# Performance work log

Hardware: AMD Instinct MI355X
Metric: run time of the kernel (lower is better)

The kernel has to match this reference:

```python
import jax, jax.numpy as jnp
import numpy as np

B, T, IN, OUT = 8, 2048, 1024, 512
DT, TAU = 1.0, 20.0


def setup_inputs() -> dict:
    key = jax.random.key(0)
    k1, k2 = jax.random.split(key)
    x = jax.random.normal(k1, (B, T, IN), jnp.float32)
    lim = 1.0 / np.sqrt(IN)
    weight = jax.random.uniform(k2, (OUT, IN), jnp.float32, -lim, lim)
    bias = jnp.zeros((OUT,), jnp.float32)
    # fixed tau trainer: decay = exp(-dt / tau) per output feature
    decay = jnp.full((OUT,), float(np.exp(-DT / TAU)), jnp.float32)
    return {"input_tensor": x, "weight": weight, "bias": bias, "decay": decay}


def reference(input_tensor, weight, bias, decay):
    # Hoist the time-invariant GEMM out of the recurrence: [B,T,OUT]
    current = jnp.einsum('bti,oi->bto', input_tensor, weight) + bias
    v0 = jnp.zeros((input_tensor.shape[0], weight.shape[0]), input_tensor.dtype)

    def step(v_tm1, c_t):
        v_t = decay * v_tm1 + (1.0 - decay) * c_t
        return v_t, v_t

    # scan over time axis: [T,B,OUT]
    _, outs = jax.lax.scan(step, v0, jnp.swapaxes(current, 0, 1))
    outputs = jnp.swapaxes(outs, 0, 1)  # [B,T,OUT]
    states = jnp.concatenate([v0[:, None, :], outputs], axis=1)[None]  # [1,B,T+1,OUT]
    return outputs, states
```

## Files before the change

### kernel.cpp

```cpp
#include <hip/hip_runtime.h>
#include <hip/hip_bf16.h>
#include <cstddef>
#include <cstdint>

#define BB    8
#define TT    2048
#define KIN   1024
#define NOUT  512
#define CHUNK 32
#define NCHUNK (TT / CHUNK)

#define BM 128
#define BN 128
#define BK 64
#define NKSTEP (KIN / BK)
#define NPAGE  (KIN / 32)
#define TILEB 8192

typedef __attribute__((ext_vector_type(4))) float          f32x4;
typedef __attribute__((ext_vector_type(4))) unsigned int   u32x4;
typedef _Float16 f16x8 __attribute__((ext_vector_type(8)));

__global__ __launch_bounds__(256) void conv_tiled_f16(
    const float* __restrict__ src, unsigned char* __restrict__ dst, int total) {
  int idx = blockIdx.x * blockDim.x + threadIdx.x;
  const int stride = gridDim.x * blockDim.x;
  for (; idx < total; idx += stride) {
    const int r  = idx >> 7;
    const int s8 = idx & 127;
    const float* p = src + (size_t)r * KIN + s8 * 8;
    float4 a = *reinterpret_cast<const float4*>(p);
    float4 b = *reinterpret_cast<const float4*>(p + 4);
    f16x8 h;
    h[0] = (_Float16)a.x; h[1] = (_Float16)a.y;
    h[2] = (_Float16)a.z; h[3] = (_Float16)a.w;
    h[4] = (_Float16)b.x; h[5] = (_Float16)b.y;
    h[6] = (_Float16)b.z; h[7] = (_Float16)b.w;
    const int row  = r & 127;
    const int page = (r >> 7) * NPAGE + (s8 >> 2);
    const int slot = (s8 & 3) ^ ((row >> 1) & 3);
    *reinterpret_cast<f16x8*>(dst + (size_t)page * TILEB + row * 64 + slot * 16) = h;
  }
}

#define G2L(gp, sp)                                                        \
  __builtin_amdgcn_global_load_lds(                                       \
      (const __attribute__((address_space(1))) void*)(gp),                \
      (__attribute__((address_space(3))) void*)(sp), 16, 0, 0)

__global__ __launch_bounds__(256, 2) void gemm_f16(
    const float* __restrict__ X, const unsigned char* __restrict__ Wt,
    const float* __restrict__ bias, const float* __restrict__ decay,
    unsigned short* __restrict__ Cws, float* __restrict__ vend) {
  __shared__ __align__(16) unsigned char smem[32768 + 16384];

  const int tid  = threadIdx.x;
  const int wave = tid >> 6;
  const int lane = tid & 63;
  const int m0 = blockIdx.x * BM;
  const int n0 = blockIdx.y * BN;
  const int wm = (wave >> 1) * 64;
  const int wn = (wave & 1) * 64;
  const int frow = lane & 15;
  const int g    = lane >> 4;

  unsigned char* sA = smem;
  unsigned char* sB = smem + 32768;

  const int arow4 = wave * 4 + (lane >> 4);
  const int aslot = lane & 15;
  const float* gA = X + (size_t)(m0 + arow4) * KIN + ((aslot ^ (arow4 & 7)) << 2);
  const int ldsw = wave * 1024;

  const unsigned char* srcB = Wt + (size_t)(n0 >> 7) * NPAGE * TILEB + tid * 16;

  const int arswz = frow & 7;
  const int swzr  = (g ^ ((frow >> 1) & 3)) << 4;

  f32x4 acc[4][4] = {};

  for (int t = 0; t < NKSTEP; ++t) {
    __syncthreads();
    const int k0 = t * BK;
#pragma unroll
    for (int q = 0; q < 8; ++q)
      G2L(gA + (size_t)(q * 16) * KIN + k0, sA + q * 4096 + ldsw);
    const size_t boff = (size_t)(2 * t) * TILEB;
#pragma unroll
    for (int q = 0; q < 4; ++q)
      G2L(srcB + boff + q * 4096, sB + q * 4096 + ldsw);
    __syncthreads();

#pragma unroll
    for (int kk = 0; kk < 2; ++kk) {
      f16x8 af[4];
#pragma unroll
      for (int mi = 0; mi < 4; ++mi) {
        const int row = wm + mi * 16 + frow;
        const unsigned char* ap = sA + row * 256;
        const int ks0 = kk * 8 + g * 2;
        f32x4 q0 = *reinterpret_cast<const f32x4*>(ap + ((ks0    ) ^ arswz) * 16);
        f32x4 q1 = *reinterpret_cast<const f32x4*>(ap + ((ks0 + 1) ^ arswz) * 16);
        u32x4 hv;
        hv[0] = __builtin_bit_cast(unsigned int, __builtin_amdgcn_cvt_pkrtz(q0[0], q0[1]));
        hv[1] = __builtin_bit_cast(unsigned int, __builtin_amdgcn_cvt_pkrtz(q0[2], q0[3]));
        hv[2] = __builtin_bit_cast(unsigned int, __builtin_amdgcn_cvt_pkrtz(q1[0], q1[1]));
        hv[3] = __builtin_bit_cast(unsigned int, __builtin_amdgcn_cvt_pkrtz(q1[2], q1[3]));
        af[mi] = __builtin_bit_cast(f16x8, hv);
      }
#pragma unroll
      for (int ni = 0; ni < 4; ++ni) {
        f16x8 bf = *reinterpret_cast<const f16x8*>(
            sB + kk * 8192 + (wn + ni * 16 + frow) * 64 + swzr);
#pragma unroll
        for (int mi = 0; mi < 4; ++mi)
          acc[mi][ni] = __builtin_amdgcn_mfma_f32_16x16x32_f16(af[mi], bf, acc[mi][ni], 0, 0, 0);
      }
    }
  }

  const int colb = n0 + wn + frow;
  const int rowb = m0 + wm + (g << 2);
  float bv[4];
#pragma unroll
  for (int ni = 0; ni < 4; ++ni) bv[ni] = bias[colb + ni * 16];
#pragma unroll
  for (int mi = 0; mi < 4; ++mi) {
#pragma unroll
    for (int r = 0; r < 4; ++r) {
#pragma unroll
      for (int ni = 0; ni < 4; ++ni) {
        const _Float16 hv = (_Float16)(acc[mi][ni][r] + bv[ni]);
        Cws[(size_t)(rowb + mi * 16 + r) * NOUT + colb + ni * 16] =
            __builtin_bit_cast(unsigned short, hv);
      }
    }
  }

  {
    float rlo[4], rhi[4];
#pragma unroll
    for (int ni = 0; ni < 4; ++ni) {
      const float d  = decay[colb + ni * 16];
      const float bb = bv[ni];
      const float omd = 1.0f - d;
      const float dd = d * d, d4 = dd * dd, d8 = d4 * d4;
      const float d16 = d8 * d8, d12 = d8 * d4;
      const float dpg = (g == 0) ? d12 : (g == 1) ? d8 : (g == 2) ? d4 : 1.0f;
      float s[4];
#pragma unroll
      for (int mi = 0; mi < 4; ++mi) {
        float v = acc[mi][ni][0] + bb;
        v = v * d + (acc[mi][ni][1] + bb);
        v = v * d + (acc[mi][ni][2] + bb);
        v = v * d + (acc[mi][ni][3] + bb);
        s[mi] = omd * v;
      }
      float ulo = dpg * (s[0] * d16 + s[1]);
      float uhi = dpg * (s[2] * d16 + s[3]);
      ulo += __shfl_xor(ulo, 16); ulo += __shfl_xor(ulo, 32);
      uhi += __shfl_xor(uhi, 16); uhi += __shfl_xor(uhi, 32);
      rlo[ni] = ulo; rhi[ni] = uhi;
    }
    const int b   = m0 >> 11;
    const int clo = ((m0 & (TT - 1)) >> 5) + (wm >> 5);
    const int chunk = clo + (g >> 1);
    const int half  = g >> 1;
    const int nia   = g & 1;
    const float v1 = half ? (nia ? rhi[1] : rhi[0]) : (nia ? rlo[1] : rlo[0]);
    const float v2 = half ? (nia ? rhi[3] : rhi[2]) : (nia ? rlo[3] : rlo[2]);
    const int col1 = n0 + wn + frow + nia * 16;
    float* vp = vend + ((size_t)b * NCHUNK + chunk) * NOUT;
    vp[col1]      = v1;
    vp[col1 + 32] = v2;
  }
}

__global__ __launch_bounds__(256) void gemm_f32_64x64(
    const float* __restrict__ X, const float* __restrict__ W,
    const float* __restrict__ bias, float* __restrict__ C) {
  __shared__ float As[16][65];
  __shared__ float Bs[16][65];
  const int m0  = blockIdx.y * 64;
  const int n0  = blockIdx.x * 64;
  const int tid = threadIdx.x;
  const int tx  = tid & 15;
  const int ty  = tid >> 4;
  const int lr  = tid >> 2;
  const int lk  = (tid & 3) << 2;
  float acc[4][4] = {};
  const float* xa = X + (size_t)(m0 + lr) * KIN + lk;
  const float* wb = W + (size_t)(n0 + lr) * KIN + lk;
  for (int k0 = 0; k0 < KIN; k0 += 16) {
    float4 av = *reinterpret_cast<const float4*>(xa + k0);
    float4 bv = *reinterpret_cast<const float4*>(wb + k0);
    As[lk + 0][lr] = av.x; As[lk + 1][lr] = av.y;
    As[lk + 2][lr] = av.z; As[lk + 3][lr] = av.w;
    Bs[lk + 0][lr] = bv.x; Bs[lk + 1][lr] = bv.y;
    Bs[lk + 2][lr] = bv.z; Bs[lk + 3][lr] = bv.w;
    __syncthreads();
#pragma unroll
    for (int k = 0; k < 16; ++k) {
      float a[4], b[4];
#pragma unroll
      for (int i = 0; i < 4; ++i) a[i] = As[k][ty * 4 + i];
#pragma unroll
      for (int j = 0; j < 4; ++j) b[j] = Bs[k][tx * 4 + j];
#pragma unroll
      for (int i = 0; i < 4; ++i)
#pragma unroll
        for (int j = 0; j < 4; ++j) acc[i][j] += a[i] * b[j];
    }
    __syncthreads();
  }
  const int n = n0 + tx * 4;
  float4 bv = *reinterpret_cast<const float4*>(&bias[n]);
#pragma unroll
  for (int i = 0; i < 4; ++i) {
    const int m = m0 + ty * 4 + i;
    float4 r;
    r.x = acc[i][0] + bv.x; r.y = acc[i][1] + bv.y;
    r.z = acc[i][2] + bv.z; r.w = acc[i][3] + bv.w;
    *reinterpret_cast<float4*>(&C[(size_t)m * NOUT + n]) = r;
  }
}

__global__ __launch_bounds__(512) void scan_fixup2(
    const unsigned short* __restrict__ Cws, const float* __restrict__ vend,
    const float* __restrict__ decay, float* __restrict__ out,
    float* __restrict__ states) {
  const int b = blockIdx.x / NCHUNK;
  const int c = blockIdx.x % NCHUNK;
  const int o = threadIdx.x;
  const float d   = decay[o];
  const float omd = 1.0f - d;
  const float dd = d * d, d4 = dd * dd, d8 = d4 * d4, d16 = d8 * d8;
  const float dL = d16 * d16;

  float v = 0.0f;
  const float* vp = vend + (size_t)b * NCHUNK * NOUT + o;
  for (int cc = 0; cc < c; ++cc) v = dL * v + vp[(size_t)cc * NOUT];

  size_t obase = ((size_t)b * TT + (size_t)c * CHUNK) * NOUT + o;
  size_t sbase = ((size_t)b * (TT + 1) + (size_t)c * CHUNK + 1) * NOUT + o;
#pragma unroll 4
  for (int k = 0; k < CHUNK; ++k) {
    const unsigned short hu = Cws[obase + (size_t)k * NOUT];
    const float cur = (float)__builtin_bit_cast(_Float16, hu);
    v = d * v + omd * cur;
    out[obase + (size_t)k * NOUT]    = v;
    states[sbase + (size_t)k * NOUT] = v;
  }
  if (c == 0) states[((size_t)b * (TT + 1)) * NOUT + o] = 0.0f;
}

__global__ __launch_bounds__(512) void scan_seq(
    float* __restrict__ C, float* __restrict__ states,
    const float* __restrict__ decay) {
  const int b = blockIdx.x;
  const int o = threadIdx.x;
  const float d   = decay[o];
  const float omd = 1.0f - d;
  float v = 0.0f;
  states[((size_t)b * (TT + 1)) * NOUT + o] = 0.0f;
  for (int t = 0; t < TT; ++t) {
    const size_t oi = ((size_t)b * TT + t) * NOUT + o;
    float x = C[oi];
    v = d * v + omd * x;
    C[oi] = v;
    states[((size_t)b * (TT + 1) + t + 1) * NOUT + o] = v;
  }
}

extern "C" void kernel_launch(void* const* d_in, const int* in_sizes, int n_in,
                              void* d_out, int out_size, void* d_ws, size_t ws_size,
                              hipStream_t stream) {
  const float* x     = (const float*)d_in[0];
  const float* w     = (const float*)d_in[1];
  const float* bias  = (const float*)d_in[2];
  const float* decay = (const float*)d_in[3];

  float* out    = (float*)d_out;
  float* states = out + (size_t)BB * TT * NOUT;

  const size_t szWb = (size_t)NOUT * KIN * sizeof(_Float16);
  const size_t szCb = (size_t)BB * TT * NOUT * sizeof(_Float16);
  const size_t scan_elems = (size_t)BB * NCHUNK * NOUT;
  const size_t need = szWb + szCb + scan_elems * sizeof(float);

  if (ws_size >= need) {
    unsigned char*  Wt   = (unsigned char*)d_ws;
    unsigned short* Cws  = (unsigned short*)(Wt + szWb);
    float*          vend = (float*)(Cws + (size_t)BB * TT * NOUT);

    conv_tiled_f16<<<256, 256, 0, stream>>>(w, Wt, NOUT * (KIN / 8));
    gemm_f16<<<dim3((BB * TT) / BM, NOUT / BN), 256, 0, stream>>>(
        x, Wt, bias, decay, Cws, vend);
    scan_fixup2<<<BB * NCHUNK, NOUT, 0, stream>>>(Cws, vend, decay, out, states);
  } else {
    gemm_f32_64x64<<<dim3(NOUT / 64, (BB * TT) / 64), 256, 0, stream>>>(x, w, bias, out);
    scan_seq<<<BB, NOUT, 0, stream>>>(out, states, decay);
  }
}
```

Before: 62.16 us.

## Fuse GEMM and chunked scan into one cooperative kernel with grid sync

Merges the GEMM and the scan fixup into a single cooperative kernel. After each tile writes its chunk-end partial sums, a grid-wide sync runs, and each wave then computes its chunk prefix and finishes the recurrence straight from accumulators staged in LDS. This removes the fp16 intermediate round trip through global memory and one kernel launch. In exchange it needs all 512 blocks co-resident (128x4 grid at 2 blocks/CU with 64KB LDS), adds a grid barrier, and serialises 64 timesteps per lane with strided stores. If the cooperative launch fails, it falls back to the old two-kernel path.

```diff
diff --git a/kernel.cpp b/kernel.cpp
--- a/kernel.cpp
+++ b/kernel.cpp
@@ -1,7 +1,10 @@
 #include <hip/hip_runtime.h>
+#include <hip/hip_cooperative_groups.h>
 #include <hip/hip_bf16.h>
 #include <cstddef>
 #include <cstdint>
+
+namespace cg = cooperative_groups;
 
 #define BB    8
 #define TT    2048
@@ -48,11 +51,12 @@
       (const __attribute__((address_space(1))) void*)(gp),                \
       (__attribute__((address_space(3))) void*)(sp), 16, 0, 0)
 
-__global__ __launch_bounds__(256, 2) void gemm_f16(
+__global__ __launch_bounds__(256, 2) void fused_gemm_scan(
     const float* __restrict__ X, const unsigned char* __restrict__ Wt,
     const float* __restrict__ bias, const float* __restrict__ decay,
-    unsigned short* __restrict__ Cws, float* __restrict__ vend) {
-  __shared__ __align__(16) unsigned char smem[32768 + 16384];
+    float* __restrict__ out, float* __restrict__ states,
+    float* __restrict__ vend) {
+  __shared__ __align__(16) unsigned char smem[65536];
 
   const int tid  = threadIdx.x;
   const int wave = tid >> 6;
@@ -120,21 +124,13 @@
   }
 
   const int colb = n0 + wn + frow;
-  const int rowb = m0 + wm + (g << 2);
-  float bv[4];
-#pragma unroll
-  for (int ni = 0; ni < 4; ++ni) bv[ni] = bias[colb + ni * 16];
-#pragma unroll
-  for (int mi = 0; mi < 4; ++mi) {
-#pragma unroll
-    for (int r = 0; r < 4; ++r) {
-#pragma unroll
-      for (int ni = 0; ni < 4; ++ni) {
-        const _Float16 hv = (_Float16)(acc[mi][ni][r] + bv[ni]);
-        Cws[(size_t)(rowb + mi * 16 + r) * NOUT + colb + ni * 16] =
-            __builtin_bit_cast(unsigned short, hv);
-      }
-    }
+#pragma unroll
+  for (int ni = 0; ni < 4; ++ni) {
+    const float bv = bias[colb + ni * 16];
+#pragma unroll
+    for (int mi = 0; mi < 4; ++mi)
+#pragma unroll
+      for (int r = 0; r < 4; ++r) acc[mi][ni][r] += bv;
   }
 
   {
@@ -142,7 +138,6 @@
 #pragma unroll
     for (int ni = 0; ni < 4; ++ni) {
       const float d  = decay[colb + ni * 16];
-      const float bb = bv[ni];
       const float omd = 1.0f - d;
       const float dd = d * d, d4 = dd * dd, d8 = d4 * d4;
       const float d16 = d8 * d8, d12 = d8 * d4;
@@ -150,10 +145,10 @@
       float s[4];
 #pragma unroll
       for (int mi = 0; mi < 4; ++mi) {
-        float v = acc[mi][ni][0] + bb;
-        v = v * d + (acc[mi][ni][1] + bb);
-        v = v * d + (acc[mi][ni][2] + bb);
-        v = v * d + (acc[mi][ni][3] + bb);
+        float v = acc[mi][ni][0];
+        v = v * d + acc[mi][ni][1];
+        v = v * d + acc[mi][ni][2];
+        v = v * d + acc[mi][ni][3];
         s[mi] = omd * v;
       }
       float ulo = dpg * (s[0] * d16 + s[1]);
@@ -174,6 +169,186 @@
     vp[col1]      = v1;
     vp[col1 + 32] = v2;
   }
+
+  cg::this_grid().sync();
+
+  float* smf = reinterpret_cast<float*>(smem) + wave * 4096;
+#pragma unroll
+  for (int mi = 0; mi < 4; ++mi)
+#pragma unroll
+    for (int r = 0; r < 4; ++r)
+#pragma unroll
+      for (int ni = 0; ni < 4; ++ni)
+        smf[(mi * 16 + g * 4 + r) * 64 + ni * 16 + frow] = acc[mi][ni][r];
+  __syncthreads();
+
+  {
+    const int col = n0 + wn + lane;
+    const float d   = decay[col];
+    const float omd = 1.0f - d;
+    const float dd = d * d, d4 = dd * dd, d8 = d4 * d4, d16 = d8 * d8;
+    const float dL = d16 * d16;
+    const int b      = m0 >> 11;
+    const int trow   = (m0 & (TT - 1)) + wm;
+    const int chunk0 = trow >> 5;
+
+    float v = 0.0f;
+    const float* vp = vend + (size_t)b * NCHUNK * NOUT + col;
+    for (int cc = 0; cc < chunk0; ++cc) v = dL * v + vp[(size_t)cc * NOUT];
+
+    size_t oidx = ((size_t)b * TT + trow) * NOUT + col;
+    size_t sidx = ((size_t)b * (TT + 1) + trow + 1) * NOUT + col;
+    for (int j = 0; j < 64; ++j) {
+      v = d * v + omd * smf[j * 64 + lane];
+      out[oidx]    = v;
+      states[sidx] = v;
+      oidx += NOUT; sidx += NOUT;
+    }
+    if (trow == 0) states[((size_t)b * (TT + 1)) * NOUT + col] = 0.0f;
+  }
+}
+
+__global__ __launch_bounds__(256, 2) void gemm_f16(
+    const float* __restrict__ X, const unsigned char* __restrict__ Wt,
+    const float* __restrict__ bias, const float* __restrict__ decay,
+    unsigned short* __restrict__ Cws, float* __restrict__ vend) {
+  __shared__ __align__(16) unsigned char smem[32768 + 16384];
+  const int tid  = threadIdx.x;
+  const int wave = tid >> 6;
+  const int lane = tid & 63;
+  const int m0 = blockIdx.x * BM;
+  const int n0 = blockIdx.y * BN;
+  const int wm = (wave >> 1) * 64;
+  const int wn = (wave & 1) * 64;
+  const int frow = lane & 15;
+  const int g    = lane >> 4;
+  unsigned char* sA = smem;
+  unsigned char* sB = smem + 32768;
+  const int arow4 = wave * 4 + (lane >> 4);
+  const int aslot = lane & 15;
+  const float* gA = X + (size_t)(m0 + arow4) * KIN + ((aslot ^ (arow4 & 7)) << 2);
+  const int ldsw = wave * 1024;
+  const unsigned char* srcB = Wt + (size_t)(n0 >> 7) * NPAGE * TILEB + tid * 16;
+  const int arswz = frow & 7;
+  const int swzr  = (g ^ ((frow >> 1) & 3)) << 4;
+  f32x4 acc[4][4] = {};
+  for (int t = 0; t < NKSTEP; ++t) {
+    __syncthreads();
+    const int k0 = t * BK;
+#pragma unroll
+    for (int q = 0; q < 8; ++q)
+      G2L(gA + (size_t)(q * 16) * KIN + k0, sA + q * 4096 + ldsw);
+    const size_t boff = (size_t)(2 * t) * TILEB;
+#pragma unroll
+    for (int q = 0; q < 4; ++q)
+      G2L(srcB + boff + q * 4096, sB + q * 4096 + ldsw);
+    __syncthreads();
+#pragma unroll
+    for (int kk = 0; kk < 2; ++kk) {
+      f16x8 af[4];
+#pragma unroll
+      for (int mi = 0; mi < 4; ++mi) {
+        const int row = wm + mi * 16 + frow;
+        const unsigned char* ap = sA + row * 256;
+        const int ks0 = kk * 8 + g * 2;
+        f32x4 q0 = *reinterpret_cast<const f32x4*>(ap + ((ks0    ) ^ arswz) * 16);
+        f32x4 q1 = *reinterpret_cast<const f32x4*>(ap + ((ks0 + 1) ^ arswz) * 16);
+        u32x4 hv;
+        hv[0] = __builtin_bit_cast(unsigned int, __builtin_amdgcn_cvt_pkrtz(q0[0], q0[1]));
+        hv[1] = __builtin_bit_cast(unsigned int, __builtin_amdgcn_cvt_pkrtz(q0[2], q0[3]));
+        hv[2] = __builtin_bit_cast(unsigned int, __builtin_amdgcn_cvt_pkrtz(q1[0], q1[1]));
+        hv[3] = __builtin_bit_cast(unsigned int, __builtin_amdgcn_cvt_pkrtz(q1[2], q1[3]));
+        af[mi] = __builtin_bit_cast(f16x8, hv);
+      }
+#pragma unroll
+      for (int ni = 0; ni < 4; ++ni) {
+        f16x8 bf = *reinterpret_cast<const f16x8*>(
+            sB + kk * 8192 + (wn + ni * 16 + frow) * 64 + swzr);
+#pragma unroll
+        for (int mi = 0; mi < 4; ++mi)
+          acc[mi][ni] = __builtin_amdgcn_mfma_f32_16x16x32_f16(af[mi], bf, acc[mi][ni], 0, 0, 0);
+      }
+    }
+  }
+  const int colb = n0 + wn + frow;
+  const int rowb = m0 + wm + (g << 2);
+  float bv[4];
+#pragma unroll
+  for (int ni = 0; ni < 4; ++ni) bv[ni] = bias[colb + ni * 16];
+#pragma unroll
+  for (int mi = 0; mi < 4; ++mi)
+#pragma unroll
+    for (int r = 0; r < 4; ++r)
+#pragma unroll
+      for (int ni = 0; ni < 4; ++ni) {
+        const _Float16 hv = (_Float16)(acc[mi][ni][r] + bv[ni]);
+        Cws[(size_t)(rowb + mi * 16 + r) * NOUT + colb + ni * 16] =
+            __builtin_bit_cast(unsigned short, hv);
+      }
+  {
+    float rlo[4], rhi[4];
+#pragma unroll
+    for (int ni = 0; ni < 4; ++ni) {
+      const float d  = decay[colb + ni * 16];
+      const float bb = bv[ni];
+      const float omd = 1.0f - d;
+      const float dd = d * d, d4 = dd * dd, d8 = d4 * d4;
+      const float d16 = d8 * d8, d12 = d8 * d4;
+      const float dpg = (g == 0) ? d12 : (g == 1) ? d8 : (g == 2) ? d4 : 1.0f;
+      float s[4];
+#pragma unroll
+      for (int mi = 0; mi < 4; ++mi) {
+        float v = acc[mi][ni][0] + bb;
+        v = v * d + (acc[mi][ni][1] + bb);
+        v = v * d + (acc[mi][ni][2] + bb);
+        v = v * d + (acc[mi][ni][3] + bb);
+        s[mi] = omd * v;
+      }
+      float ulo = dpg * (s[0] * d16 + s[1]);
+      float uhi = dpg * (s[2] * d16 + s[3]);
+      ulo += __shfl_xor(ulo, 16); ulo += __shfl_xor(ulo, 32);
+      uhi += __shfl_xor(uhi, 16); uhi += __shfl_xor(uhi, 32);
+      rlo[ni] = ulo; rhi[ni] = uhi;
+    }
+    const int b   = m0 >> 11;
+    const int clo = ((m0 & (TT - 1)) >> 5) + (wm >> 5);
+    const int chunk = clo + (g >> 1);
+    const int half  = g >> 1;
+    const int nia   = g & 1;
+    const float v1 = half ? (nia ? rhi[1] : rhi[0]) : (nia ? rlo[1] : rlo[0]);
+    const float v2 = half ? (nia ? rhi[3] : rhi[2]) : (nia ? rlo[3] : rlo[2]);
+    const int col1 = n0 + wn + frow + nia * 16;
+    float* vp = vend + ((size_t)b * NCHUNK + chunk) * NOUT;
+    vp[col1]      = v1;
+    vp[col1 + 32] = v2;
+  }
+}
+
+__global__ __launch_bounds__(512) void scan_fixup2(
+    const unsigned short* __restrict__ Cws, const float* __restrict__ vend,
+    const float* __restrict__ decay, float* __restrict__ out,
+    float* __restrict__ states) {
+  const int b = blockIdx.x / NCHUNK;
+  const int c = blockIdx.x % NCHUNK;
+  const int o = threadIdx.x;
+  const float d   = decay[o];
+  const float omd = 1.0f - d;
+  const float dd = d * d, d4 = dd * dd, d8 = d4 * d4, d16 = d8 * d8;
+  const float dL = d16 * d16;
+  float v = 0.0f;
+  const float* vp = vend + (size_t)b * NCHUNK * NOUT + o;
+  for (int cc = 0; cc < c; ++cc) v = dL * v + vp[(size_t)cc * NOUT];
+  size_t obase = ((size_t)b * TT + (size_t)c * CHUNK) * NOUT + o;
+  size_t sbase = ((size_t)b * (TT + 1) + (size_t)c * CHUNK + 1) * NOUT + o;
+#pragma unroll 4
+  for (int k = 0; k < CHUNK; ++k) {
+    const unsigned short hu = Cws[obase + (size_t)k * NOUT];
+    const float cur = (float)__builtin_bit_cast(_Float16, hu);
+    v = d * v + omd * cur;
+    out[obase + (size_t)k * NOUT]    = v;
+    states[sbase + (size_t)k * NOUT] = v;
+  }
+  if (c == 0) states[((size_t)b * (TT + 1)) * NOUT + o] = 0.0f;
 }
 
 __global__ __launch_bounds__(256) void gemm_f32_64x64(
@@ -225,35 +400,6 @@
   }
 }
 
-__global__ __launch_bounds__(512) void scan_fixup2(
-    const unsigned short* __restrict__ Cws, const float* __restrict__ vend,
-    const float* __restrict__ decay, float* __restrict__ out,
-    float* __restrict__ states) {
-  const int b = blockIdx.x / NCHUNK;
-  const int c = blockIdx.x % NCHUNK;
-  const int o = threadIdx.x;
-  const float d   = decay[o];
-  const float omd = 1.0f - d;
-  const float dd = d * d, d4 = dd * dd, d8 = d4 * d4, d16 = d8 * d8;
-  const float dL = d16 * d16;
-
-  float v = 0.0f;
-  const float* vp = vend + (size_t)b * NCHUNK * NOUT + o;
-  for (int cc = 0; cc < c; ++cc) v = dL * v + vp[(size_t)cc * NOUT];
-
-  size_t obase = ((size_t)b * TT + (size_t)c * CHUNK) * NOUT + o;
-  size_t sbase = ((size_t)b * (TT + 1) + (size_t)c * CHUNK + 1) * NOUT + o;
-#pragma unroll 4
-  for (int k = 0; k < CHUNK; ++k) {
-    const unsigned short hu = Cws[obase + (size_t)k * NOUT];
-    const float cur = (float)__builtin_bit_cast(_Float16, hu);
-    v = d * v + omd * cur;
-    out[obase + (size_t)k * NOUT]    = v;
-    states[sbase + (size_t)k * NOUT] = v;
-  }
-  if (c == 0) states[((size_t)b * (TT + 1)) * NOUT + o] = 0.0f;
-}
-
 __global__ __launch_bounds__(512) void scan_seq(
     float* __restrict__ C, float* __restrict__ states,
     const float* __restrict__ decay) {
@@ -284,19 +430,28 @@
   float* states = out + (size_t)BB * TT * NOUT;
 
   const size_t szWb = (size_t)NOUT * KIN * sizeof(_Float16);
+  const size_t scan_elems = (size_t)BB * NCHUNK * NOUT;
+  const size_t szVd = scan_elems * sizeof(float);
   const size_t szCb = (size_t)BB * TT * NOUT * sizeof(_Float16);
-  const size_t scan_elems = (size_t)BB * NCHUNK * NOUT;
-  const size_t need = szWb + szCb + scan_elems * sizeof(float);
+  const size_t need = szWb + szVd + szCb;
 
   if (ws_size >= need) {
     unsigned char*  Wt   = (unsigned char*)d_ws;
-    unsigned short* Cws  = (unsigned short*)(Wt + szWb);
-    float*          vend = (float*)(Cws + (size_t)BB * TT * NOUT);
+    float*          vend = (float*)(Wt + szWb);
+    unsigned short* Cws  = (unsigned short*)((unsigned char*)d_ws + szWb + szVd);
 
     conv_tiled_f16<<<256, 256, 0, stream>>>(w, Wt, NOUT * (KIN / 8));
-    gemm_f16<<<dim3((BB * TT) / BM, NOUT / BN), 256, 0, stream>>>(
-        x, Wt, bias, decay, Cws, vend);
-    scan_fixup2<<<BB * NCHUNK, NOUT, 0, stream>>>(Cws, vend, decay, out, states);
+
+    void* args[] = {(void*)&x, (void*)&Wt, (void*)&bias, (void*)&decay,
+                    (void*)&out, (void*)&states, (void*)&vend};
+    hipError_t err = hipLaunchCooperativeKernel(
+        reinterpret_cast<void*>(fused_gemm_scan),
+        dim3((BB * TT) / BM, NOUT / BN), dim3(256), args, 0, stream);
+    if (err != hipSuccess) {
+      gemm_f16<<<dim3((BB * TT) / BM, NOUT / BN), 256, 0, stream>>>(
+          x, Wt, bias, decay, Cws, vend);
+      scan_fixup2<<<BB * NCHUNK, NOUT, 0, stream>>>(Cws, vend, decay, out, states);
+    }
   } else {
     gemm_f32_64x64<<<dim3(NOUT / 64, (BB * TT) / 64), 256, 0, stream>>>(x, w, bias, out);
     scan_seq<<<BB, NOUT, 0, stream>>>(out, states, decay);
```

Measured after the change: 120.8 us. 94.3% more time.

## Double-buffer GEMM LDS tiles with BK=32 to overlap loads and MFMA

Applied to the files above, without the earlier changes.

The GEMM main loop now uses two LDS buffers with a K-step of 32, issuing the async global-to-LDS loads for the next step before computing on the current one. This replaces the load, sync, compute, sync pattern, so global latency can hide behind MFMA work and only one barrier is needed per step. The trade-off is twice as many iterations with less work each. LDS per block stays at 48KB. Correctness relies on the async loads having completed at the single barrier, and the A-tile address remapping has to match the new 128-byte row layout.

```diff
diff --git a/kernel.cpp b/kernel.cpp
--- a/kernel.cpp
+++ b/kernel.cpp
@@ -12,10 +12,11 @@
 
 #define BM 128
 #define BN 128
-#define BK 64
+#define BK 32
 #define NKSTEP (KIN / BK)
 #define NPAGE  (KIN / 32)
 #define TILEB 8192
+#define BUFB  24576
 
 typedef __attribute__((ext_vector_type(4))) float          f32x4;
 typedef __attribute__((ext_vector_type(4))) unsigned int   u32x4;
@@ -52,7 +53,7 @@
     const float* __restrict__ X, const unsigned char* __restrict__ Wt,
     const float* __restrict__ bias, const float* __restrict__ decay,
     unsigned short* __restrict__ Cws, float* __restrict__ vend) {
-  __shared__ __align__(16) unsigned char smem[32768 + 16384];
+  __shared__ __align__(16) unsigned char smem[2 * BUFB];
 
   const int tid  = threadIdx.x;
   const int wave = tid >> 6;
@@ -64,12 +65,9 @@
   const int frow = lane & 15;
   const int g    = lane >> 4;
 
-  unsigned char* sA = smem;
-  unsigned char* sB = smem + 32768;
-
-  const int arow4 = wave * 4 + (lane >> 4);
-  const int aslot = lane & 15;
-  const float* gA = X + (size_t)(m0 + arow4) * KIN + ((aslot ^ (arow4 & 7)) << 2);
+  const int arow  = tid >> 3;
+  const int aslot = tid & 7;
+  const float* gA = X + (size_t)(m0 + arow) * KIN + ((aslot ^ (arow & 7)) << 2);
   const int ldsw = wave * 1024;
 
   const unsigned char* srcB = Wt + (size_t)(n0 >> 7) * NPAGE * TILEB + tid * 16;
@@ -79,44 +77,50 @@
 
   f32x4 acc[4][4] = {};
 
+  auto stage = [&](unsigned char* buf, int t) {
+    const int k0 = t * BK;
+#pragma unroll
+    for (int q = 0; q < 4; ++q)
+      G2L(gA + (size_t)(q * 32) * KIN + k0, buf + q * 4096 + ldsw);
+    const size_t boff = (size_t)t * TILEB;
+    G2L(srcB + boff,        buf + 16384 + ldsw);
+    G2L(srcB + boff + 4096, buf + 16384 + 4096 + ldsw);
+  };
+
+  stage(smem, 0);
+  __syncthreads();
+
   for (int t = 0; t < NKSTEP; ++t) {
+    unsigned char* cur = smem + (t & 1) * BUFB;
+    unsigned char* nxt = smem + ((t + 1) & 1) * BUFB;
+
+    if (t + 1 < NKSTEP) stage(nxt, t + 1);
+
+    f16x8 af[4];
+#pragma unroll
+    for (int mi = 0; mi < 4; ++mi) {
+      const int row = wm + mi * 16 + frow;
+      const unsigned char* ap = cur + row * 128;
+      const int s0 = g * 2;
+      f32x4 q0 = *reinterpret_cast<const f32x4*>(ap + ((s0)     ^ arswz) * 16);
+      f32x4 q1 = *reinterpret_cast<const f32x4*>(ap + ((s0 + 1) ^ arswz) * 16);
+      u32x4 hv;
+      hv[0] = __builtin_bit_cast(unsigned int, __builtin_amdgcn_cvt_pkrtz(q0[0], q0[1]));
+      hv[1] = __builtin_bit_cast(unsigned int, __builtin_amdgcn_cvt_pkrtz(q0[2], q0[3]));
+      hv[2] = __builtin_bit_cast(unsigned int, __builtin_amdgcn_cvt_pkrtz(q1[0], q1[1]));
+      hv[3] = __builtin_bit_cast(unsigned int, __builtin_amdgcn_cvt_pkrtz(q1[2], q1[3]));
+      af[mi] = __builtin_bit_cast(f16x8, hv);
+    }
+#pragma unroll
+    for (int ni = 0; ni < 4; ++ni) {
+      f16x8 bf = *reinterpret_cast<const f16x8*>(
+          cur + 16384 + (wn + ni * 16 + frow) * 64 + swzr);
+#pragma unroll
+      for (int mi = 0; mi < 4; ++mi)
+        acc[mi][ni] = __builtin_amdgcn_mfma_f32_16x16x32_f16(af[mi], bf, acc[mi][ni], 0, 0, 0);
+    }
+
     __syncthreads();
-    const int k0 = t * BK;
-#pragma unroll
-    for (int q = 0; q < 8; ++q)
-      G2L(gA + (size_t)(q * 16) * KIN + k0, sA + q * 4096 + ldsw);
-    const size_t boff = (size_t)(2 * t) * TILEB;
-#pragma unroll
-    for (int q = 0; q < 4; ++q)
-      G2L(srcB + boff + q * 4096, sB + q * 4096 + ldsw);
-    __syncthreads();
-
-#pragma unroll
-    for (int kk = 0; kk < 2; ++kk) {
-      f16x8 af[4];
-#pragma unroll
-      for (int mi = 0; mi < 4; ++mi) {
-        const int row = wm + mi * 16 + frow;
-        const unsigned char* ap = sA + row * 256;
-        const int ks0 = kk * 8 + g * 2;
-        f32x4 q0 = *reinterpret_cast<const f32x4*>(ap + ((ks0    ) ^ arswz) * 16);
-        f32x4 q1 = *reinterpret_cast<const f32x4*>(ap + ((ks0 + 1) ^ arswz) * 16);
-        u32x4 hv;
-        hv[0] = __builtin_bit_cast(unsigned int, __builtin_amdgcn_cvt_pkrtz(q0[0], q0[1]));
-        hv[1] = __builtin_bit_cast(unsigned int, __builtin_amdgcn_cvt_pkrtz(q0[2], q0[3]));
-        hv[2] = __builtin_bit_cast(unsigned int, __builtin_amdgcn_cvt_pkrtz(q1[0], q1[1]));
-        hv[3] = __builtin_bit_cast(unsigned int, __builtin_amdgcn_cvt_pkrtz(q1[2], q1[3]));
-        af[mi] = __builtin_bit_cast(f16x8, hv);
-      }
-#pragma unroll
-      for (int ni = 0; ni < 4; ++ni) {
-        f16x8 bf = *reinterpret_cast<const f16x8*>(
-            sB + kk * 8192 + (wn + ni * 16 + frow) * 64 + swzr);
-#pragma unroll
-        for (int mi = 0; mi < 4; ++mi)
-          acc[mi][ni] = __builtin_amdgcn_mfma_f32_16x16x32_f16(af[mi], bf, acc[mi][ni], 0, 0, 0);
-      }
-    }
   }
 
   const int colb = n0 + wn + frow;
```

Result: no change. 61.94 us (-0.3%).
